# Kernel optimization log

Hardware: AMD Instinct MI355X
Metric: run time of the kernel (lower is better)

Reference implementation:

```python
import jax, jax.numpy as jnp
import numpy as np

B, N, NODE_DIM = 8, 128, 64
L, RES_DIM = 512, 1024
CG, CP = 128, 128
NUM_GNN_STEPS = 3
HID = CG + CP // 2  # interaction hidden = 192


def setup_inputs() -> dict:
    key = jax.random.key(0)
    ks = jax.random.split(key, 20)
    a = (jax.random.uniform(ks[0], (B, N, N)) < 0.05).astype(jnp.float32)
    adj = jnp.clip(a + jnp.swapaxes(a, 1, 2), 0.0, 1.0)
    adj = adj * (1.0 - jnp.eye(N, dtype=jnp.float32))
    nodes = jax.random.normal(ks[1], (B, N, NODE_DIM), dtype=jnp.float32)
    prot = jax.random.normal(ks[2], (B, L, RES_DIM), dtype=jnp.float32)
    s = 0.02
    inp = {
        "adj_mats": adj, "nodes": nodes, "protein_sequences": prot,
        "Wn": jax.random.normal(ks[3], (NODE_DIM, CG)) * s, "bn": jnp.zeros((CG,)),
        "Wg": jax.random.normal(ks[4], (CG, CG)) * s, "bg": jnp.zeros((CG,)),
        "Wr": jax.random.normal(ks[5], (RES_DIM, CP)) * s, "br": jnp.zeros((CP,)),
        "Wa": jax.random.normal(ks[6], (CG + CP, 1)) * s, "ba": jnp.zeros((1,)),
        "W1": jax.random.normal(ks[7], (CG + CP, HID)) * s, "b1": jnp.zeros((HID,)),
        "W2": jax.random.normal(ks[8], (HID, CG)) * s, "b2": jnp.zeros((CG,)),
        "Wo": jax.random.normal(ks[9], (CG, 1)) * s, "bo": jnp.zeros((1,)),
    }
    return inp


def reference(adj_mats, nodes, protein_sequences,
              Wn, bn, Wg, bg, Wr, br, Wa, ba, W1, b1, W2, b2, Wo, bo):
    # node compression: [B,N,CG]
    h = nodes @ Wn + bn
    deg = jnp.clip(jnp.sum(adj_mats, axis=-1), 1.0, None)        # [B,N]
    norm = deg ** -0.5                                           # [B,N]
    for i in range(NUM_GNN_STEPS):
        m = jnp.einsum('bij,bjc->bic', adj_mats, h * norm[..., None])
        h = (m * norm[..., None]) @ Wg + bg
        h = jnp.tanh(h) if i == NUM_GNN_STEPS - 1 else jax.nn.relu(h)
    # residue compression: [B,L,CP]
    r = protein_sequences @ Wr + br
    # MergeSnE1: all-pairs broadcast concat -> [B, N*L, CG+CP]
    cat = jnp.concatenate([
        jnp.broadcast_to(h[:, :, None, :], (B, N, L, CG)),
        jnp.broadcast_to(r[:, None, :, :], (B, N, L, CP)),
    ], axis=-1).reshape(B, N * L, CG + CP)
    # attention: Linear -> Softmax over last dim (size 1 => all ones, faithful)
    attn = jax.nn.softmax(cat @ Wa + ba, axis=-1)                # [B,N*L,1]
    inter = jax.nn.relu(cat @ W1 + b1) @ W2 + b2                 # [B,N*L,CG]
    weighted_sum = jnp.sum(attn * inter, axis=1)                 # [B,CG]
    return weighted_sum @ Wo + bo                                # [B,1]
```

## Files before the change

kernel.cpp:

```cpp
#include <hip/hip_runtime.h>
#include <hip/hip_bf16.h>

#define BB 8
#define NN 128
#define ND 64
#define LL 512
#define RD 1024
#define CG 128
#define HID 192

typedef __attribute__((ext_vector_type(8))) short short8;
typedef __attribute__((ext_vector_type(4))) float f32x4;

__device__ __forceinline__ unsigned short f2bf(float x) {
    return __bfloat16_as_ushort(__float2bfloat16(x));
}
__device__ __forceinline__ float bf2f(unsigned short h) {
    unsigned u = ((unsigned)h) << 16;
    return __builtin_bit_cast(float, u);
}
__device__ __forceinline__ float fast_tanh(float x) {
    float e = __expf(2.0f * x);
    return 1.0f - 2.0f * __builtin_amdgcn_rcpf(e + 1.0f);
}
#define MFMA __builtin_amdgcn_mfma_f32_16x16x32_bf16

__global__ __launch_bounds__(512, 1) void k_prep(
    const float* __restrict__ adj, const float* __restrict__ nodes,
    const float* __restrict__ Wn, const float* __restrict__ bn,
    const float* __restrict__ Wr, const float* __restrict__ br,
    const float* __restrict__ W1, const float* __restrict__ b1,
    const float* __restrict__ Wg, const float* __restrict__ bg,
    const float* __restrict__ W2, const float* __restrict__ b2,
    const float* __restrict__ Wo, const float* __restrict__ bo,
    unsigned short* __restrict__ WcT, unsigned short* __restrict__ hW1b,
    float* __restrict__ vbuf, float* __restrict__ out)
{
    __shared__ unsigned short hT[NN][136];
    __shared__ unsigned short mbuf[NN][72];
    __shared__ unsigned short WgT[NN][136];
    __shared__ unsigned short W1T[HID][136];
    __shared__ float snorm[NN];
    __shared__ float b1cL[HID];
    __shared__ float sbg[NN];
    int t = threadIdx.x, blk = blockIdx.x;
    int w = t >> 6, l = t & 63, lr = l & 15, ks = l >> 4, lk = ks * 8;
    const float* W1b = W1 + CG * HID;

    if (blk < 16) {
        int r0 = blk * 64;
        #pragma unroll
        for (int q = 0; q < 48; ++q) {
            int e = t + 512 * q;
            int m = e / HID, c = e % HID;
            W1T[c][m] = f2bf(W1[(size_t)(CG + m) * HID + c]);
        }
        int rt = w & 3, jh = w >> 2;
        short8 awr[4];
        #pragma unroll
        for (int kk = 0; kk < 4; ++kk) {
            const float* wp = Wr + (size_t)(r0 + rt * 16 + lr) * CG + kk * 32 + lk;
            float4 q0 = *(const float4*)wp;
            float4 q1 = *(const float4*)(wp + 4);
            unsigned short u[8];
            u[0]=f2bf(q0.x); u[1]=f2bf(q0.y); u[2]=f2bf(q0.z); u[3]=f2bf(q0.w);
            u[4]=f2bf(q1.x); u[5]=f2bf(q1.y); u[6]=f2bf(q1.z); u[7]=f2bf(q1.w);
            awr[kk] = *(const short8*)u;
        }
        __syncthreads();
        #pragma unroll
        for (int jt6 = 0; jt6 < 6; ++jt6) {
            int jt = jh * 6 + jt6;
            f32x4 d = {0.f, 0.f, 0.f, 0.f};
            #pragma unroll
            for (int kk = 0; kk < 4; ++kk) {
                short8 bf = *(const short8*)(&W1T[jt * 16 + lr][kk * 32 + lk]);
                d = MFMA(awr[kk], bf, d, 0, 0, 0);
            }
            unsigned short u[4];
            #pragma unroll
            for (int i = 0; i < 4; ++i) u[i] = f2bf(d[i]);
            *(uint2*)(WcT + (size_t)(jt * 16 + lr) * RD + r0 + rt * 16 + ks * 4) = *(uint2*)u;
        }
        return;
    }
    if (blk == 16) {
        if (t < HID) {
            float s = 0.f;
            #pragma unroll 8
            for (int k = 0; k < CG; ++k) s = fmaf(W2[t * CG + k], Wo[k], s);
            vbuf[t] = s;
        }
        if (t < BB) {
            float s = 0.f;
            for (int k = 0; k < CG; ++k) s = fmaf(b2[k], Wo[k], s);
            out[t] = (float)(NN * LL) * s + bo[0];
        }
        return;
    }

    int b = blk - 17;
    int i0 = w * 16;

    {
        float* dscr = (float*)&mbuf[0][0];
        int row = t >> 2, q4 = t & 3;
        const float* ar = adj + ((size_t)b * NN + row) * NN + q4 * 32;
        float d = 0.f;
        #pragma unroll
        for (int c4 = 0; c4 < 8; ++c4) {
            float4 p = *(const float4*)(ar + c4 * 4);
            d += (p.x + p.y) + (p.z + p.w);
        }
        dscr[row * 4 + q4] = d;
        __syncthreads();
        if (t < NN) {
            snorm[t] = rsqrtf(fmaxf(dscr[t*4] + dscr[t*4+1] + dscr[t*4+2] + dscr[t*4+3], 1.f));
        } else if (t < 320) {
            int j = t - 128;
            float s = b1[j];
            #pragma unroll 8
            for (int m = 0; m < CG; ++m)
                s = fmaf(br[m], W1b[(size_t)m * HID + j], s);
            b1cL[j] = s;
        } else if (t < 448) {
            sbg[t - 320] = bg[t - 320];
        }
        __syncthreads();
    }

    unsigned short* WnT = &mbuf[0][0];
    #pragma unroll
    for (int q = 0; q < 16; ++q) {
        int e = t + 512 * q;
        int c = e & 127, k = e >> 7;
        WnT[c * 72 + k] = f2bf(Wn[(size_t)k * CG + c]);
    }
    #pragma unroll
    for (int q = 0; q < 32; ++q) {
        int e = t + 512 * q;
        int c = e & 127, j = e >> 7;
        WgT[c][j] = f2bf(Wg[(size_t)j * CG + c]);
    }
    #pragma unroll
    for (int q = 0; q < 32; ++q) {
        int e = t + 512 * q;
        int jj = e & 127, k = e >> 7;
        W1T[jj][k] = f2bf(W1[(size_t)k * HID + jj]);
    }
    #pragma unroll
    for (int q = 0; q < 16; ++q) {
        int e = t + 512 * q;
        int jj = 128 + (e & 63), k = e >> 6;
        W1T[jj][k] = f2bf(W1[(size_t)k * HID + jj]);
    }

    short8 af[4];
    {
        float ni = snorm[i0 + lr];
        const float* ar = adj + ((size_t)b * NN + i0 + lr) * NN;
        #pragma unroll
        for (int kk = 0; kk < 4; ++kk) {
            int kb = kk * 32 + lk;
            float4 p0 = *(const float4*)(ar + kb);
            float4 p1 = *(const float4*)(ar + kb + 4);
            unsigned short u[8];
            u[0] = f2bf(p0.x * ni * snorm[kb+0]); u[1] = f2bf(p0.y * ni * snorm[kb+1]);
            u[2] = f2bf(p0.z * ni * snorm[kb+2]); u[3] = f2bf(p0.w * ni * snorm[kb+3]);
            u[4] = f2bf(p1.x * ni * snorm[kb+4]); u[5] = f2bf(p1.y * ni * snorm[kb+5]);
            u[6] = f2bf(p1.z * ni * snorm[kb+6]); u[7] = f2bf(p1.w * ni * snorm[kb+7]);
            af[kk] = *(const short8*)u;
        }
    }
    short8 bnod[2];
    #pragma unroll
    for (int kk = 0; kk < 2; ++kk) {
        const float* np = nodes + ((size_t)b * NN + i0 + lr) * ND + kk * 32 + lk;
        float4 q0 = *(const float4*)np;
        float4 q1 = *(const float4*)(np + 4);
        unsigned short u[8];
        u[0]=f2bf(q0.x); u[1]=f2bf(q0.y); u[2]=f2bf(q0.z); u[3]=f2bf(q0.w);
        u[4]=f2bf(q1.x); u[5]=f2bf(q1.y); u[6]=f2bf(q1.z); u[7]=f2bf(q1.w);
        bnod[kk] = *(const short8*)u;
    }
    __syncthreads();

    #pragma unroll
    for (int ct = 0; ct < 8; ++ct) {
        f32x4 d = {0.f, 0.f, 0.f, 0.f};
        #pragma unroll
        for (int kk = 0; kk < 2; ++kk) {
            short8 afw = *(const short8*)(WnT + (ct * 16 + lr) * 72 + kk * 32 + lk);
            d = MFMA(afw, bnod[kk], d, 0, 0, 0);
        }
        #pragma unroll
        for (int i = 0; i < 4; ++i)
            hT[ct * 16 + ks * 4 + i][i0 + lr] = f2bf(d[i] + bn[ct * 16 + ks * 4 + i]);
    }
    __syncthreads();

    for (int s = 0; s < 3; ++s) {
        f32x4 acc8[8];
        #pragma unroll
        for (int ct = 0; ct < 8; ++ct) acc8[ct] = (f32x4){0.f, 0.f, 0.f, 0.f};
        #pragma unroll
        for (int hf = 0; hf < 2; ++hf) {
            #pragma unroll
            for (int jt = 0; jt < 4; ++jt) {
                int jg = hf * 64 + jt * 16;
                f32x4 d = {0.f, 0.f, 0.f, 0.f};
                #pragma unroll
                for (int kk = 0; kk < 4; ++kk) {
                    short8 bf = *(const short8*)(&hT[jg + lr][kk * 32 + lk]);
                    d = MFMA(af[kk], bf, d, 0, 0, 0);
                }
                #pragma unroll
                for (int i = 0; i < 4; ++i)
                    mbuf[i0 + ks * 4 + i][jt * 16 + lr] = f2bf(d[i]);
            }
            short8 bm[2];
            #pragma unroll
            for (int kk = 0; kk < 2; ++kk)
                bm[kk] = *(const short8*)(&mbuf[i0 + lr][kk * 32 + lk]);
            #pragma unroll
            for (int ct = 0; ct < 8; ++ct) {
                #pragma unroll
                for (int kk = 0; kk < 2; ++kk) {
                    short8 wf = *(const short8*)(&WgT[ct * 16 + lr][hf * 64 + kk * 32 + lk]);
                    if (s < 2)
                        acc8[ct] = MFMA(wf, bm[kk], acc8[ct], 0, 0, 0);
                    else
                        acc8[ct] = MFMA(bm[kk], wf, acc8[ct], 0, 0, 0);
                }
            }
        }
        __syncthreads();
        if (s < 2) {
            #pragma unroll
            for (int ct = 0; ct < 8; ++ct)
                #pragma unroll
                for (int i = 0; i < 4; ++i)
                    hT[ct * 16 + ks * 4 + i][i0 + lr] =
                        f2bf(fmaxf(acc8[ct][i] + sbg[ct * 16 + ks * 4 + i], 0.f));
        } else {
            #pragma unroll
            for (int ct = 0; ct < 8; ++ct)
                #pragma unroll
                for (int i = 0; i < 4; ++i)
                    hT[i0 + ks * 4 + i][ct * 16 + lr] =
                        f2bf(fast_tanh(acc8[ct][i] + sbg[ct * 16 + lr]));
        }
        __syncthreads();
    }

    {
        short8 bh[4];
        #pragma unroll
        for (int kk = 0; kk < 4; ++kk)
            bh[kk] = *(const short8*)(&hT[i0 + lr][kk * 32 + lk]);
        #pragma unroll
        for (int jjt = 0; jjt < 12; ++jjt) {
            f32x4 d = {0.f, 0.f, 0.f, 0.f};
            #pragma unroll
            for (int kk = 0; kk < 4; ++kk) {
                short8 wf = *(const short8*)(&W1T[jjt * 16 + lr][kk * 32 + lk]);
                d = MFMA(wf, bh[kk], d, 0, 0, 0);
            }
            #pragma unroll
            for (int i = 0; i < 4; ++i) {
                int jj = jjt * 16 + ks * 4 + i;
                hW1b[(size_t)b * HID * NN + jj * NN + i0 + lr] = f2bf(d[i] + b1cL[jj]);
            }
        }
    }
}

__global__ __launch_bounds__(512, 4) void k_gemm(
    const float* __restrict__ prot, const unsigned short* __restrict__ WcT,
    const unsigned short* __restrict__ hW1b, const float* __restrict__ vbuf,
    float* __restrict__ out)
{
    __shared__ unsigned short aT[16 * 1032];
    __shared__ unsigned short h1[HID * 136];
    __shared__ float pbuf[2 * 16 * 192];
    __shared__ float sred[8];
    int t = threadIdx.x, blk = blockIdx.x;
    int b = blk >> 5, lc = blk & 31;
    int w = t >> 6, l = t & 63, lr = l & 15, ks = l >> 4, lk = ks * 8;
    int w2 = w >> 2, wj = w & 3;

    #pragma unroll
    for (int q = 0; q < 4; ++q) {
        int e = t + 512 * q;
        int row = e >> 7;
        int c8 = (e & 127) * 8;
        const float* pr = prot + ((size_t)(b * LL + lc * 16 + row)) * RD + c8;
        float4 p0 = *(const float4*)pr;
        float4 p1 = *(const float4*)(pr + 4);
        unsigned short u[8];
        u[0]=f2bf(p0.x); u[1]=f2bf(p0.y); u[2]=f2bf(p0.z); u[3]=f2bf(p0.w);
        u[4]=f2bf(p1.x); u[5]=f2bf(p1.y); u[6]=f2bf(p1.z); u[7]=f2bf(p1.w);
        *(short8*)(aT + row * 1032 + c8) = *(const short8*)u;
    }
    #pragma unroll
    for (int q = 0; q < 6; ++q) {
        int u8 = t + 512 * q;
        int row = u8 >> 4;
        int n8 = (u8 & 15) * 8;
        short8 v = *(const short8*)(hW1b + (size_t)b * HID * NN + row * NN + n8);
        *(short8*)(h1 + row * 136 + n8) = v;
    }
    float v0 = vbuf[wj * 48 + lr];
    float v1 = vbuf[wj * 48 + 16 + lr];
    float v2 = vbuf[wj * 48 + 32 + lr];
    __syncthreads();

    f32x4 a0 = {0.f,0.f,0.f,0.f}, a1 = a0, a2 = a0;
    {
        const unsigned short* ap = aT + lr * 1032 + w2 * 512 + lk;
        const unsigned short* bp = WcT + (size_t)(wj * 48 + lr) * RD + w2 * 512 + lk;
        #pragma unroll 4
        for (int k0 = 0; k0 < 512; k0 += 32) {
            short8 av = *(const short8*)(ap + k0);
            short8 b0 = *(const short8*)(bp + k0);
            short8 b1 = *(const short8*)(bp + 16 * RD + k0);
            short8 b2 = *(const short8*)(bp + 32 * RD + k0);
            a0 = MFMA(av, b0, a0, 0, 0, 0);
            a1 = MFMA(av, b1, a1, 0, 0, 0);
            a2 = MFMA(av, b2, a2, 0, 0, 0);
        }
    }
    #pragma unroll
    for (int i = 0; i < 4; ++i) {
        int r = ks * 4 + i;
        pbuf[(w2 * 16 + r) * 192 + wj * 48 + lr]      = a0[i];
        pbuf[(w2 * 16 + r) * 192 + wj * 48 + 16 + lr] = a1[i];
        pbuf[(w2 * 16 + r) * 192 + wj * 48 + 32 + lr] = a2[i];
    }
    __syncthreads();
    float rw0[4], rw1[4], rw2[4];
    #pragma unroll
    for (int i = 0; i < 4; ++i) {
        int r = ks * 4 + i;
        rw0[i] = pbuf[r * 192 + wj*48 + lr]      + pbuf[(16 + r) * 192 + wj*48 + lr];
        rw1[i] = pbuf[r * 192 + wj*48 + 16 + lr] + pbuf[(16 + r) * 192 + wj*48 + 16 + lr];
        rw2[i] = pbuf[r * 192 + wj*48 + 32 + lr] + pbuf[(16 + r) * 192 + wj*48 + 32 + lr];
    }

    const unsigned short* h0p = h1 + (wj * 48 + lr) * 136 + w2 * 64;
    const unsigned short* h1p = h0p + 16 * 136;
    const unsigned short* h2p = h0p + 32 * 136;
    float s = 0.f;
    #pragma unroll 2
    for (int n0 = 0; n0 < 64; n0 += 4) {
        unsigned short e0[4], e1[4], e2[4];
        *(uint2*)e0 = *(const uint2*)(h0p + n0);
        *(uint2*)e1 = *(const uint2*)(h1p + n0);
        *(uint2*)e2 = *(const uint2*)(h2p + n0);
        #pragma unroll
        for (int q = 0; q < 4; ++q) {
            float hh0 = bf2f(e0[q]), hh1 = bf2f(e1[q]), hh2 = bf2f(e2[q]);
            #pragma unroll
            for (int i = 0; i < 4; ++i) {
                s = fmaf(v0, fmaxf(rw0[i] + hh0, 0.f), s);
                s = fmaf(v1, fmaxf(rw1[i] + hh1, 0.f), s);
                s = fmaf(v2, fmaxf(rw2[i] + hh2, 0.f), s);
            }
        }
    }
    for (int off = 32; off; off >>= 1) s += __shfl_down(s, off);
    if (l == 0) sred[w] = s;
    __syncthreads();
    if (t == 0) {
        float tot = ((sred[0] + sred[1]) + (sred[2] + sred[3]))
                  + ((sred[4] + sred[5]) + (sred[6] + sred[7]));
        atomicAdd(&out[b], tot);
    }
}

extern "C" void kernel_launch(void* const* d_in, const int* in_sizes, int n_in,
                              void* d_out, int out_size, void* d_ws, size_t ws_size,
                              hipStream_t stream)
{
    const float* adj   = (const float*)d_in[0];
    const float* nodes = (const float*)d_in[1];
    const float* prot  = (const float*)d_in[2];
    const float* Wn    = (const float*)d_in[3];
    const float* bn    = (const float*)d_in[4];
    const float* Wg    = (const float*)d_in[5];
    const float* bg    = (const float*)d_in[6];
    const float* Wr    = (const float*)d_in[7];
    const float* br    = (const float*)d_in[8];
    const float* W1    = (const float*)d_in[11];
    const float* b1    = (const float*)d_in[12];
    const float* W2    = (const float*)d_in[13];
    const float* b2    = (const float*)d_in[14];
    const float* Wo    = (const float*)d_in[15];
    const float* bo    = (const float*)d_in[16];

    float* ws     = (float*)d_ws;
    float* vbuf   = ws;
    unsigned short* hW1b = (unsigned short*)(ws + 192);
    unsigned short* WcT  = hW1b + (size_t)BB * HID * NN;
    float* out    = (float*)d_out;

    hipLaunchKernelGGL(k_prep, dim3(25), dim3(512), 0, stream,
                       adj, nodes, Wn, bn, Wr, br, W1, b1, Wg, bg,
                       W2, b2, Wo, bo, WcT, hW1b, vbuf, out);
    hipLaunchKernelGGL(k_gemm, dim3(256), dim3(512), 0, stream,
                       prot, WcT, hW1b, vbuf, out);
}
```

Before: 53.43 us.

## Double k_prep block size to 1024 threads and split GNN work across wave halves

k_prep now launches 1024 threads per block. In the per-batch blocks each 16-row tile is shared by two waves that split output columns, and in the Wr×W1 blocks the 16 waves split the output tiles. The GNN step is restructured: both halves write the full 128-wide message tile to a widened mbuf, sync once, then each wave computes half of the Wg output columns. The intent is to shorten the serial latency of the small prep kernel with more waves per CU, at the cost of more LDS and a larger block that runs one per CU.

Result: no change. 53.56 us (+0.2%).

```diff
diff --git a/kernel.cpp b/kernel.cpp
--- a/kernel.cpp
+++ b/kernel.cpp
@@ -25,7 +25,7 @@
 }
 #define MFMA __builtin_amdgcn_mfma_f32_16x16x32_bf16
 
-__global__ __launch_bounds__(512, 1) void k_prep(
+__global__ __launch_bounds__(1024, 1) void k_prep(
     const float* __restrict__ adj, const float* __restrict__ nodes,
     const float* __restrict__ Wn, const float* __restrict__ bn,
     const float* __restrict__ Wr, const float* __restrict__ br,
@@ -37,7 +37,7 @@
     float* __restrict__ vbuf, float* __restrict__ out)
 {
     __shared__ unsigned short hT[NN][136];
-    __shared__ unsigned short mbuf[NN][72];
+    __shared__ unsigned short mbuf[NN][136];
     __shared__ unsigned short WgT[NN][136];
     __shared__ unsigned short W1T[HID][136];
     __shared__ float snorm[NN];
@@ -50,12 +50,12 @@
     if (blk < 16) {
         int r0 = blk * 64;
         #pragma unroll
-        for (int q = 0; q < 48; ++q) {
-            int e = t + 512 * q;
+        for (int q = 0; q < 24; ++q) {
+            int e = t + 1024 * q;
             int m = e / HID, c = e % HID;
             W1T[c][m] = f2bf(W1[(size_t)(CG + m) * HID + c]);
         }
-        int rt = w & 3, jh = w >> 2;
+        int rt = w & 3, jq = w >> 2;
         short8 awr[4];
         #pragma unroll
         for (int kk = 0; kk < 4; ++kk) {
@@ -69,8 +69,8 @@
         }
         __syncthreads();
         #pragma unroll
-        for (int jt6 = 0; jt6 < 6; ++jt6) {
-            int jt = jh * 6 + jt6;
+        for (int jt3 = 0; jt3 < 3; ++jt3) {
+            int jt = jq * 3 + jt3;
             f32x4 d = {0.f, 0.f, 0.f, 0.f};
             #pragma unroll
             for (int kk = 0; kk < 4; ++kk) {
@@ -100,22 +100,25 @@
     }
 
     int b = blk - 17;
-    int i0 = w * 16;
+    int wi = w & 7, wh = w >> 3;
+    int i0 = wi * 16;
 
     {
         float* dscr = (float*)&mbuf[0][0];
-        int row = t >> 2, q4 = t & 3;
-        const float* ar = adj + ((size_t)b * NN + row) * NN + q4 * 32;
+        int row = t >> 3, q8 = t & 7;
+        const float* ar = adj + ((size_t)b * NN + row) * NN + q8 * 16;
         float d = 0.f;
         #pragma unroll
-        for (int c4 = 0; c4 < 8; ++c4) {
+        for (int c4 = 0; c4 < 4; ++c4) {
             float4 p = *(const float4*)(ar + c4 * 4);
             d += (p.x + p.y) + (p.z + p.w);
         }
-        dscr[row * 4 + q4] = d;
+        dscr[row * 8 + q8] = d;
         __syncthreads();
         if (t < NN) {
-            snorm[t] = rsqrtf(fmaxf(dscr[t*4] + dscr[t*4+1] + dscr[t*4+2] + dscr[t*4+3], 1.f));
+            float dd = ((dscr[t*8+0] + dscr[t*8+1]) + (dscr[t*8+2] + dscr[t*8+3]))
+                     + ((dscr[t*8+4] + dscr[t*8+5]) + (dscr[t*8+6] + dscr[t*8+7]));
+            snorm[t] = rsqrtf(fmaxf(dd, 1.f));
         } else if (t < 320) {
             int j = t - 128;
             float s = b1[j];
@@ -131,26 +134,26 @@
 
     unsigned short* WnT = &mbuf[0][0];
     #pragma unroll
-    for (int q = 0; q < 16; ++q) {
-        int e = t + 512 * q;
+    for (int q = 0; q < 8; ++q) {
+        int e = t + 1024 * q;
         int c = e & 127, k = e >> 7;
         WnT[c * 72 + k] = f2bf(Wn[(size_t)k * CG + c]);
     }
     #pragma unroll
-    for (int q = 0; q < 32; ++q) {
-        int e = t + 512 * q;
+    for (int q = 0; q < 16; ++q) {
+        int e = t + 1024 * q;
         int c = e & 127, j = e >> 7;
         WgT[c][j] = f2bf(Wg[(size_t)j * CG + c]);
     }
     #pragma unroll
-    for (int q = 0; q < 32; ++q) {
-        int e = t + 512 * q;
+    for (int q = 0; q < 16; ++q) {
+        int e = t + 1024 * q;
         int jj = e & 127, k = e >> 7;
         W1T[jj][k] = f2bf(W1[(size_t)k * HID + jj]);
     }
     #pragma unroll
-    for (int q = 0; q < 16; ++q) {
-        int e = t + 512 * q;
+    for (int q = 0; q < 8; ++q) {
+        int e = t + 1024 * q;
         int jj = 128 + (e & 63), k = e >> 6;
         W1T[jj][k] = f2bf(W1[(size_t)k * HID + jj]);
     }
@@ -186,69 +189,62 @@
     __syncthreads();
 
     #pragma unroll
-    for (int ct = 0; ct < 8; ++ct) {
+    for (int ct = 0; ct < 4; ++ct) {
+        int ctp = wh * 4 + ct;
         f32x4 d = {0.f, 0.f, 0.f, 0.f};
         #pragma unroll
         for (int kk = 0; kk < 2; ++kk) {
-            short8 afw = *(const short8*)(WnT + (ct * 16 + lr) * 72 + kk * 32 + lk);
+            short8 afw = *(const short8*)(WnT + (ctp * 16 + lr) * 72 + kk * 32 + lk);
             d = MFMA(afw, bnod[kk], d, 0, 0, 0);
         }
         #pragma unroll
         for (int i = 0; i < 4; ++i)
-            hT[ct * 16 + ks * 4 + i][i0 + lr] = f2bf(d[i] + bn[ct * 16 + ks * 4 + i]);
+            hT[ctp * 16 + ks * 4 + i][i0 + lr] = f2bf(d[i] + bn[ctp * 16 + ks * 4 + i]);
     }
     __syncthreads();
 
     for (int s = 0; s < 3; ++s) {
-        f32x4 acc8[8];
-        #pragma unroll
-        for (int ct = 0; ct < 8; ++ct) acc8[ct] = (f32x4){0.f, 0.f, 0.f, 0.f};
-        #pragma unroll
-        for (int hf = 0; hf < 2; ++hf) {
-            #pragma unroll
-            for (int jt = 0; jt < 4; ++jt) {
-                int jg = hf * 64 + jt * 16;
-                f32x4 d = {0.f, 0.f, 0.f, 0.f};
-                #pragma unroll
-                for (int kk = 0; kk < 4; ++kk) {
-                    short8 bf = *(const short8*)(&hT[jg + lr][kk * 32 + lk]);
-                    d = MFMA(af[kk], bf, d, 0, 0, 0);
-                }
+        #pragma unroll
+        for (int jt = 0; jt < 4; ++jt) {
+            int jg = wh * 64 + jt * 16;
+            f32x4 d = {0.f, 0.f, 0.f, 0.f};
+            #pragma unroll
+            for (int kk = 0; kk < 4; ++kk) {
+                short8 bf = *(const short8*)(&hT[jg + lr][kk * 32 + lk]);
+                d = MFMA(af[kk], bf, d, 0, 0, 0);
+            }
+            #pragma unroll
+            for (int i = 0; i < 4; ++i)
+                mbuf[i0 + ks * 4 + i][jg + lr] = f2bf(d[i]);
+        }
+        __syncthreads();
+        short8 bm[4];
+        #pragma unroll
+        for (int kk = 0; kk < 4; ++kk)
+            bm[kk] = *(const short8*)(&mbuf[i0 + lr][kk * 32 + lk]);
+        #pragma unroll
+        for (int ct = 0; ct < 4; ++ct) {
+            int ctp = wh * 4 + ct;
+            f32x4 acc = {0.f, 0.f, 0.f, 0.f};
+            #pragma unroll
+            for (int kk = 0; kk < 4; ++kk) {
+                short8 wf = *(const short8*)(&WgT[ctp * 16 + lr][kk * 32 + lk]);
+                if (s < 2)
+                    acc = MFMA(wf, bm[kk], acc, 0, 0, 0);
+                else
+                    acc = MFMA(bm[kk], wf, acc, 0, 0, 0);
+            }
+            if (s < 2) {
                 #pragma unroll
                 for (int i = 0; i < 4; ++i)
-                    mbuf[i0 + ks * 4 + i][jt * 16 + lr] = f2bf(d[i]);
-            }
-            short8 bm[2];
-            #pragma unroll
-            for (int kk = 0; kk < 2; ++kk)
-                bm[kk] = *(const short8*)(&mbuf[i0 + lr][kk * 32 + lk]);
-            #pragma unroll
-            for (int ct = 0; ct < 8; ++ct) {
-                #pragma unroll
-                for (int kk = 0; kk < 2; ++kk) {
-                    short8 wf = *(const short8*)(&WgT[ct * 16 + lr][hf * 64 + kk * 32 + lk]);
-                    if (s < 2)
-                        acc8[ct] = MFMA(wf, bm[kk], acc8[ct], 0, 0, 0);
-                    else
-                        acc8[ct] = MFMA(bm[kk], wf, acc8[ct], 0, 0, 0);
-                }
-            }
-        }
-        __syncthreads();
-        if (s < 2) {
-            #pragma unroll
-            for (int ct = 0; ct < 8; ++ct)
+                    hT[ctp * 16 + ks * 4 + i][i0 + lr] =
+                        f2bf(fmaxf(acc[i] + sbg[ctp * 16 + ks * 4 + i], 0.f));
+            } else {
                 #pragma unroll
                 for (int i = 0; i < 4; ++i)
-                    hT[ct * 16 + ks * 4 + i][i0 + lr] =
-                        f2bf(fmaxf(acc8[ct][i] + sbg[ct * 16 + ks * 4 + i], 0.f));
-        } else {
-            #pragma unroll
-            for (int ct = 0; ct < 8; ++ct)
-                #pragma unroll
-                for (int i = 0; i < 4; ++i)
-                    hT[i0 + ks * 4 + i][ct * 16 + lr] =
-                        f2bf(fast_tanh(acc8[ct][i] + sbg[ct * 16 + lr]));
+                    hT[i0 + ks * 4 + i][ctp * 16 + lr] =
+                        f2bf(fast_tanh(acc[i] + sbg[ctp * 16 + lr]));
+            }
         }
         __syncthreads();
     }
@@ -259,7 +255,8 @@
         for (int kk = 0; kk < 4; ++kk)
             bh[kk] = *(const short8*)(&hT[i0 + lr][kk * 32 + lk]);
         #pragma unroll
-        for (int jjt = 0; jjt < 12; ++jjt) {
+        for (int jt6 = 0; jt6 < 6; ++jt6) {
+            int jjt = wh * 6 + jt6;
             f32x4 d = {0.f, 0.f, 0.f, 0.f};
             #pragma unroll
             for (int kk = 0; kk < 4; ++kk) {
@@ -404,7 +401,7 @@
     unsigned short* WcT  = hW1b + (size_t)BB * HID * NN;
     float* out    = (float*)d_out;
 
-    hipLaunchKernelGGL(k_prep, dim3(25), dim3(512), 0, stream,
+    hipLaunchKernelGGL(k_prep, dim3(25), dim3(1024), 0, stream,
                        adj, nodes, Wn, bn, Wr, br, W1, b1, Wg, bg,
                        W2, b2, Wo, bo, WcT, hW1b, vbuf, out);
     hipLaunchKernelGGL(k_gemm, dim3(256), dim3(512), 0, stream,
```

## Split per-batch GNN prep into per-step kernels spread over 64 blocks

Applied to the files above, without the earlier changes.

The single prep kernel, which ran three GNN steps serially in one block per batch, is split into a setup kernel plus three step kernels. Each step kernel uses 8 blocks per batch, each handling 16 node rows. Intermediate node features ping-pong through global memory between launches. This spreads the serial GNN critical path across more compute units, at the cost of extra kernel launches, global round-trips, and each block reconverting Wg (and W1 in the final step) to bf16.

Result: slower. 55.46 us (+3.8%).

```diff
diff --git a/kernel.cpp b/kernel.cpp
--- a/kernel.cpp
+++ b/kernel.cpp
@@ -25,35 +25,76 @@
 }
 #define MFMA __builtin_amdgcn_mfma_f32_16x16x32_bf16
 
-__global__ __launch_bounds__(512, 1) void k_prep(
+__global__ __launch_bounds__(512, 1) void k1(
     const float* __restrict__ adj, const float* __restrict__ nodes,
     const float* __restrict__ Wn, const float* __restrict__ bn,
     const float* __restrict__ Wr, const float* __restrict__ br,
     const float* __restrict__ W1, const float* __restrict__ b1,
-    const float* __restrict__ Wg, const float* __restrict__ bg,
     const float* __restrict__ W2, const float* __restrict__ b2,
     const float* __restrict__ Wo, const float* __restrict__ bo,
-    unsigned short* __restrict__ WcT, unsigned short* __restrict__ hW1b,
-    float* __restrict__ vbuf, float* __restrict__ out)
+    unsigned short* __restrict__ hA, float* __restrict__ normb,
+    unsigned short* __restrict__ WcT, float* __restrict__ vbuf,
+    float* __restrict__ b1cg, float* __restrict__ out)
 {
-    __shared__ unsigned short hT[NN][136];
-    __shared__ unsigned short mbuf[NN][72];
-    __shared__ unsigned short WgT[NN][136];
-    __shared__ unsigned short W1T[HID][136];
-    __shared__ float snorm[NN];
-    __shared__ float b1cL[HID];
-    __shared__ float sbg[NN];
+    __shared__ char pool[53248];
     int t = threadIdx.x, blk = blockIdx.x;
     int w = t >> 6, l = t & 63, lr = l & 15, ks = l >> 4, lk = ks * 8;
     const float* W1b = W1 + CG * HID;
 
-    if (blk < 16) {
-        int r0 = blk * 64;
+    if (blk < 64) {
+        unsigned short* WnTl = (unsigned short*)pool;
+        float* dscr = (float*)(pool + 128 * 72 * 2);
+        int b = blk >> 3, it = blk & 7, i0 = it * 16;
+        #pragma unroll
+        for (int q = 0; q < 16; ++q) {
+            int e = t + 512 * q;
+            int c = e & 127, k = e >> 7;
+            WnTl[c * 72 + k] = f2bf(Wn[(size_t)k * CG + c]);
+        }
+        {
+            int row = t >> 5, seg = t & 31;
+            float4 p = *(const float4*)(adj + ((size_t)b * NN + i0 + row) * NN + seg * 4);
+            dscr[row * 32 + seg] = (p.x + p.y) + (p.z + p.w);
+        }
+        short8 bnod[2];
+        #pragma unroll
+        for (int kk = 0; kk < 2; ++kk) {
+            const float* np = nodes + ((size_t)b * NN + i0 + lr) * ND + kk * 32 + lk;
+            float4 q0 = *(const float4*)np;
+            float4 q1 = *(const float4*)(np + 4);
+            unsigned short u[8];
+            u[0]=f2bf(q0.x); u[1]=f2bf(q0.y); u[2]=f2bf(q0.z); u[3]=f2bf(q0.w);
+            u[4]=f2bf(q1.x); u[5]=f2bf(q1.y); u[6]=f2bf(q1.z); u[7]=f2bf(q1.w);
+            bnod[kk] = *(const short8*)u;
+        }
+        __syncthreads();
+        if (t < 16) {
+            float d = 0.f;
+            #pragma unroll
+            for (int s2 = 0; s2 < 32; ++s2) d += dscr[t * 32 + s2];
+            normb[b * NN + i0 + t] = rsqrtf(fmaxf(d, 1.f));
+        }
+        f32x4 d = {0.f, 0.f, 0.f, 0.f};
+        #pragma unroll
+        for (int kk = 0; kk < 2; ++kk) {
+            short8 afw = *(const short8*)(WnTl + (w * 16 + lr) * 72 + kk * 32 + lk);
+            d = MFMA(afw, bnod[kk], d, 0, 0, 0);
+        }
+        #pragma unroll
+        for (int i = 0; i < 4; ++i) {
+            int c = w * 16 + ks * 4 + i;
+            hA[(size_t)(b * CG + c) * NN + i0 + lr] = f2bf(d[i] + bn[c]);
+        }
+        return;
+    }
+    if (blk < 80) {
+        unsigned short (*W1Tw)[136] = (unsigned short(*)[136])pool;
+        int r0 = (blk - 64) * 64;
         #pragma unroll
         for (int q = 0; q < 48; ++q) {
             int e = t + 512 * q;
             int m = e / HID, c = e % HID;
-            W1T[c][m] = f2bf(W1[(size_t)(CG + m) * HID + c]);
+            W1Tw[c][m] = f2bf(W1[(size_t)(CG + m) * HID + c]);
         }
         int rt = w & 3, jh = w >> 2;
         short8 awr[4];
@@ -74,7 +115,7 @@
             f32x4 d = {0.f, 0.f, 0.f, 0.f};
             #pragma unroll
             for (int kk = 0; kk < 4; ++kk) {
-                short8 bf = *(const short8*)(&W1T[jt * 16 + lr][kk * 32 + lk]);
+                short8 bf = *(const short8*)(&W1Tw[jt * 16 + lr][kk * 32 + lk]);
                 d = MFMA(awr[kk], bf, d, 0, 0, 0);
             }
             unsigned short u[4];
@@ -84,80 +125,82 @@
         }
         return;
     }
-    if (blk == 16) {
-        if (t < HID) {
-            float s = 0.f;
-            #pragma unroll 8
-            for (int k = 0; k < CG; ++k) s = fmaf(W2[t * CG + k], Wo[k], s);
-            vbuf[t] = s;
-        }
-        if (t < BB) {
-            float s = 0.f;
-            for (int k = 0; k < CG; ++k) s = fmaf(b2[k], Wo[k], s);
-            out[t] = (float)(NN * LL) * s + bo[0];
-        }
-        return;
-    }
-
-    int b = blk - 17;
-    int i0 = w * 16;
-
-    {
-        float* dscr = (float*)&mbuf[0][0];
-        int row = t >> 2, q4 = t & 3;
-        const float* ar = adj + ((size_t)b * NN + row) * NN + q4 * 32;
-        float d = 0.f;
-        #pragma unroll
-        for (int c4 = 0; c4 < 8; ++c4) {
-            float4 p = *(const float4*)(ar + c4 * 4);
-            d += (p.x + p.y) + (p.z + p.w);
-        }
-        dscr[row * 4 + q4] = d;
-        __syncthreads();
-        if (t < NN) {
-            snorm[t] = rsqrtf(fmaxf(dscr[t*4] + dscr[t*4+1] + dscr[t*4+2] + dscr[t*4+3], 1.f));
-        } else if (t < 320) {
-            int j = t - 128;
-            float s = b1[j];
-            #pragma unroll 8
-            for (int m = 0; m < CG; ++m)
-                s = fmaf(br[m], W1b[(size_t)m * HID + j], s);
-            b1cL[j] = s;
-        } else if (t < 448) {
-            sbg[t - 320] = bg[t - 320];
-        }
-        __syncthreads();
-    }
-
-    unsigned short* WnT = &mbuf[0][0];
-    #pragma unroll
-    for (int q = 0; q < 16; ++q) {
-        int e = t + 512 * q;
-        int c = e & 127, k = e >> 7;
-        WnT[c * 72 + k] = f2bf(Wn[(size_t)k * CG + c]);
+    if (t < HID) {
+        float s = 0.f;
+        #pragma unroll 8
+        for (int k = 0; k < CG; ++k) s = fmaf(W2[t * CG + k], Wo[k], s);
+        vbuf[t] = s;
+    }
+    if (t < BB) {
+        float s = 0.f;
+        for (int k = 0; k < CG; ++k) s = fmaf(b2[k], Wo[k], s);
+        out[t] = (float)(NN * LL) * s + bo[0];
+    }
+    if (t >= 192 && t < 384) {
+        int j = t - 192;
+        float s = b1[j];
+        #pragma unroll 8
+        for (int m = 0; m < CG; ++m)
+            s = fmaf(br[m], W1b[(size_t)m * HID + j], s);
+        b1cg[j] = s;
+    }
+}
+
+template <int FIN>
+__global__ __launch_bounds__(512, 1) void k_step(
+    const float* __restrict__ adj, const float* __restrict__ normb,
+    const float* __restrict__ Wg, const float* __restrict__ bg,
+    const float* __restrict__ W1, const float* __restrict__ b1cg,
+    const unsigned short* __restrict__ hin, unsigned short* __restrict__ hout,
+    unsigned short* __restrict__ hW1b)
+{
+    __shared__ char pool[FIN ? 131584 : 79360];
+    unsigned short (*hTl)[136]  = (unsigned short(*)[136])(pool);
+    unsigned short (*WgTl)[136] = (unsigned short(*)[136])(pool + 34816);
+    unsigned short (*mloc)[136] = (unsigned short(*)[136])(pool + 69632);
+    unsigned short (*thl)[136]  = (unsigned short(*)[136])(pool + 73984);
+    float* snl  = (float*)(pool + 78336);
+    float* sbgl = (float*)(pool + 78848);
+    unsigned short (*W1Tl)[136] = (unsigned short(*)[136])(pool + 79360);
+
+    int t = threadIdx.x, blk = blockIdx.x;
+    int b = blk >> 3, it = blk & 7, i0 = it * 16;
+    int w = t >> 6, l = t & 63, lr = l & 15, ks = l >> 4, lk = ks * 8;
+
+    #pragma unroll
+    for (int q = 0; q < 4; ++q) {
+        int e8 = t + 512 * q;
+        int row = e8 >> 4, n8 = (e8 & 15) * 8;
+        *(short8*)(&hTl[row][n8]) =
+            *(const short8*)(hin + (size_t)(b * CG + row) * NN + n8);
     }
     #pragma unroll
     for (int q = 0; q < 32; ++q) {
         int e = t + 512 * q;
         int c = e & 127, j = e >> 7;
-        WgT[c][j] = f2bf(Wg[(size_t)j * CG + c]);
-    }
-    #pragma unroll
-    for (int q = 0; q < 32; ++q) {
-        int e = t + 512 * q;
-        int jj = e & 127, k = e >> 7;
-        W1T[jj][k] = f2bf(W1[(size_t)k * HID + jj]);
-    }
-    #pragma unroll
-    for (int q = 0; q < 16; ++q) {
-        int e = t + 512 * q;
-        int jj = 128 + (e & 63), k = e >> 6;
-        W1T[jj][k] = f2bf(W1[(size_t)k * HID + jj]);
-    }
+        WgTl[c][j] = f2bf(Wg[(size_t)j * CG + c]);
+    }
+    if (FIN) {
+        #pragma unroll
+        for (int q = 0; q < 32; ++q) {
+            int e = t + 512 * q;
+            int jj = e & 127, k = e >> 7;
+            W1Tl[jj][k] = f2bf(W1[(size_t)k * HID + jj]);
+        }
+        #pragma unroll
+        for (int q = 0; q < 16; ++q) {
+            int e = t + 512 * q;
+            int jj = 128 + (e & 63), k = e >> 6;
+            W1Tl[jj][k] = f2bf(W1[(size_t)k * HID + jj]);
+        }
+    }
+    if (t < 128) snl[t] = normb[b * NN + t];
+    else if (t < 256) sbgl[t - 128] = bg[t - 128];
+    __syncthreads();
 
     short8 af[4];
     {
-        float ni = snorm[i0 + lr];
+        float ni = snl[i0 + lr];
         const float* ar = adj + ((size_t)b * NN + i0 + lr) * NN;
         #pragma unroll
         for (int kk = 0; kk < 4; ++kk) {
@@ -165,111 +208,75 @@
             float4 p0 = *(const float4*)(ar + kb);
             float4 p1 = *(const float4*)(ar + kb + 4);
             unsigned short u[8];
-            u[0] = f2bf(p0.x * ni * snorm[kb+0]); u[1] = f2bf(p0.y * ni * snorm[kb+1]);
-            u[2] = f2bf(p0.z * ni * snorm[kb+2]); u[3] = f2bf(p0.w * ni * snorm[kb+3]);
-            u[4] = f2bf(p1.x * ni * snorm[kb+4]); u[5] = f2bf(p1.y * ni * snorm[kb+5]);
-            u[6] = f2bf(p1.z * ni * snorm[kb+6]); u[7] = f2bf(p1.w * ni * snorm[kb+7]);
+            u[0] = f2bf(p0.x * ni * snl[kb+0]); u[1] = f2bf(p0.y * ni * snl[kb+1]);
+            u[2] = f2bf(p0.z * ni * snl[kb+2]); u[3] = f2bf(p0.w * ni * snl[kb+3]);
+            u[4] = f2bf(p1.x * ni * snl[kb+4]); u[5] = f2bf(p1.y * ni * snl[kb+5]);
+            u[6] = f2bf(p1.z * ni * snl[kb+6]); u[7] = f2bf(p1.w * ni * snl[kb+7]);
             af[kk] = *(const short8*)u;
         }
     }
-    short8 bnod[2];
-    #pragma unroll
-    for (int kk = 0; kk < 2; ++kk) {
-        const float* np = nodes + ((size_t)b * NN + i0 + lr) * ND + kk * 32 + lk;
-        float4 q0 = *(const float4*)np;
-        float4 q1 = *(const float4*)(np + 4);
-        unsigned short u[8];
-        u[0]=f2bf(q0.x); u[1]=f2bf(q0.y); u[2]=f2bf(q0.z); u[3]=f2bf(q0.w);
-        u[4]=f2bf(q1.x); u[5]=f2bf(q1.y); u[6]=f2bf(q1.z); u[7]=f2bf(q1.w);
-        bnod[kk] = *(const short8*)u;
+
+    {
+        int jg = w * 16;
+        f32x4 d = {0.f, 0.f, 0.f, 0.f};
+        #pragma unroll
+        for (int kk = 0; kk < 4; ++kk) {
+            short8 bf = *(const short8*)(&hTl[jg + lr][kk * 32 + lk]);
+            d = MFMA(af[kk], bf, d, 0, 0, 0);
+        }
+        #pragma unroll
+        for (int i = 0; i < 4; ++i)
+            mloc[ks * 4 + i][jg + lr] = f2bf(d[i]);
     }
     __syncthreads();
 
-    #pragma unroll
-    for (int ct = 0; ct < 8; ++ct) {
-        f32x4 d = {0.f, 0.f, 0.f, 0.f};
-        #pragma unroll
-        for (int kk = 0; kk < 2; ++kk) {
-            short8 afw = *(const short8*)(WnT + (ct * 16 + lr) * 72 + kk * 32 + lk);
-            d = MFMA(afw, bnod[kk], d, 0, 0, 0);
+    short8 bm[4];
+    #pragma unroll
+    for (int kk = 0; kk < 4; ++kk)
+        bm[kk] = *(const short8*)(&mloc[lr][kk * 32 + lk]);
+    if (!FIN) {
+        f32x4 acc = {0.f, 0.f, 0.f, 0.f};
+        #pragma unroll
+        for (int kk = 0; kk < 4; ++kk) {
+            short8 wf = *(const short8*)(&WgTl[w * 16 + lr][kk * 32 + lk]);
+            acc = MFMA(wf, bm[kk], acc, 0, 0, 0);
+        }
+        #pragma unroll
+        for (int i = 0; i < 4; ++i) {
+            int c = w * 16 + ks * 4 + i;
+            hout[(size_t)(b * CG + c) * NN + i0 + lr] =
+                f2bf(fmaxf(acc[i] + sbgl[c], 0.f));
+        }
+    } else {
+        f32x4 acc = {0.f, 0.f, 0.f, 0.f};
+        #pragma unroll
+        for (int kk = 0; kk < 4; ++kk) {
+            short8 wf = *(const short8*)(&WgTl[w * 16 + lr][kk * 32 + lk]);
+            acc = MFMA(bm[kk], wf, acc, 0, 0, 0);
         }
         #pragma unroll
         for (int i = 0; i < 4; ++i)
-            hT[ct * 16 + ks * 4 + i][i0 + lr] = f2bf(d[i] + bn[ct * 16 + ks * 4 + i]);
-    }
-    __syncthreads();
-
-    for (int s = 0; s < 3; ++s) {
-        f32x4 acc8[8];
-        #pragma unroll
-        for (int ct = 0; ct < 8; ++ct) acc8[ct] = (f32x4){0.f, 0.f, 0.f, 0.f};
-        #pragma unroll
-        for (int hf = 0; hf < 2; ++hf) {
-            #pragma unroll
-            for (int jt = 0; jt < 4; ++jt) {
-                int jg = hf * 64 + jt * 16;
+            thl[ks * 4 + i][w * 16 + lr] = f2bf(fast_tanh(acc[i] + sbgl[w * 16 + lr]));
+        __syncthreads();
+        short8 bh[4];
+        #pragma unroll
+        for (int kk = 0; kk < 4; ++kk)
+            bh[kk] = *(const short8*)(&thl[lr][kk * 32 + lk]);
+        #pragma unroll
+        for (int q1 = 0; q1 < 2; ++q1) {
+            int jjt = w + 8 * q1;
+            if (jjt < 12) {
                 f32x4 d = {0.f, 0.f, 0.f, 0.f};
                 #pragma unroll
                 for (int kk = 0; kk < 4; ++kk) {
-                    short8 bf = *(const short8*)(&hT[jg + lr][kk * 32 + lk]);
-                    d = MFMA(af[kk], bf, d, 0, 0, 0);
+                    short8 wf = *(const short8*)(&W1Tl[jjt * 16 + lr][kk * 32 + lk]);
+                    d = MFMA(wf, bh[kk], d, 0, 0, 0);
                 }
                 #pragma unroll
-                for (int i = 0; i < 4; ++i)
-                    mbuf[i0 + ks * 4 + i][jt * 16 + lr] = f2bf(d[i]);
-            }
-            short8 bm[2];
-            #pragma unroll
-            for (int kk = 0; kk < 2; ++kk)
-                bm[kk] = *(const short8*)(&mbuf[i0 + lr][kk * 32 + lk]);
-            #pragma unroll
-            for (int ct = 0; ct < 8; ++ct) {
-                #pragma unroll
-                for (int kk = 0; kk < 2; ++kk) {
-                    short8 wf = *(const short8*)(&WgT[ct * 16 + lr][hf * 64 + kk * 32 + lk]);
-                    if (s < 2)
-                        acc8[ct] = MFMA(wf, bm[kk], acc8[ct], 0, 0, 0);
-                    else
-                        acc8[ct] = MFMA(bm[kk], wf, acc8[ct], 0, 0, 0);
+                for (int i = 0; i < 4; ++i) {
+                    int jj = jjt * 16 + ks * 4 + i;
+                    hW1b[(size_t)(b * HID + jj) * NN + i0 + lr] = f2bf(d[i] + b1cg[jj]);
                 }
-            }
-        }
-        __syncthreads();
-        if (s < 2) {
-            #pragma unroll
-            for (int ct = 0; ct < 8; ++ct)
-                #pragma unroll
-                for (int i = 0; i < 4; ++i)
-                    hT[ct * 16 + ks * 4 + i][i0 + lr] =
-                        f2bf(fmaxf(acc8[ct][i] + sbg[ct * 16 + ks * 4 + i], 0.f));
-        } else {
-            #pragma unroll
-            for (int ct = 0; ct < 8; ++ct)
-                #pragma unroll
-                for (int i = 0; i < 4; ++i)
-                    hT[i0 + ks * 4 + i][ct * 16 + lr] =
-                        f2bf(fast_tanh(acc8[ct][i] + sbg[ct * 16 + lr]));
-        }
-        __syncthreads();
-    }
-
-    {
-        short8 bh[4];
-        #pragma unroll
-        for (int kk = 0; kk < 4; ++kk)
-            bh[kk] = *(const short8*)(&hT[i0 + lr][kk * 32 + lk]);
-        #pragma unroll
-        for (int jjt = 0; jjt < 12; ++jjt) {
-            f32x4 d = {0.f, 0.f, 0.f, 0.f};
-            #pragma unroll
-            for (int kk = 0; kk < 4; ++kk) {
-                short8 wf = *(const short8*)(&W1T[jjt * 16 + lr][kk * 32 + lk]);
-                d = MFMA(wf, bh[kk], d, 0, 0, 0);
-            }
-            #pragma unroll
-            for (int i = 0; i < 4; ++i) {
-                int jj = jjt * 16 + ks * 4 + i;
-                hW1b[(size_t)b * HID * NN + jj * NN + i0 + lr] = f2bf(d[i] + b1cL[jj]);
             }
         }
     }
@@ -398,15 +405,25 @@
     const float* Wo    = (const float*)d_in[15];
     const float* bo    = (const float*)d_in[16];
 
-    float* ws     = (float*)d_ws;
-    float* vbuf   = ws;
-    unsigned short* hW1b = (unsigned short*)(ws + 192);
-    unsigned short* WcT  = hW1b + (size_t)BB * HID * NN;
-    float* out    = (float*)d_out;
-
-    hipLaunchKernelGGL(k_prep, dim3(25), dim3(512), 0, stream,
-                       adj, nodes, Wn, bn, Wr, br, W1, b1, Wg, bg,
-                       W2, b2, Wo, bo, WcT, hW1b, vbuf, out);
+    float* ws    = (float*)d_ws;
+    float* vbuf  = ws;
+    float* b1cg  = ws + 192;
+    float* normb = ws + 384;
+    unsigned short* hA   = (unsigned short*)(ws + 1408);
+    unsigned short* hB   = hA + 131072;
+    unsigned short* hW1b = hB + 131072;
+    unsigned short* WcT  = hW1b + 196608;
+    float* out   = (float*)d_out;
+
+    hipLaunchKernelGGL(k1, dim3(81), dim3(512), 0, stream,
+                       adj, nodes, Wn, bn, Wr, br, W1, b1, W2, b2, Wo, bo,
+                       hA, normb, WcT, vbuf, b1cg, out);
+    hipLaunchKernelGGL(k_step<0>, dim3(64), dim3(512), 0, stream,
+                       adj, normb, Wg, bg, W1, b1cg, hA, hB, hW1b);
+    hipLaunchKernelGGL(k_step<0>, dim3(64), dim3(512), 0, stream,
+                       adj, normb, Wg, bg, W1, b1cg, hB, hA, hW1b);
+    hipLaunchKernelGGL(k_step<1>, dim3(64), dim3(512), 0, stream,
+                       adj, normb, Wg, bg, W1, b1cg, hA, hB, hW1b);
     hipLaunchKernelGGL(k_gemm, dim3(256), dim3(512), 0, stream,
                        prot, WcT, hW1b, vbuf, out);
 }
```
